# Performance work log

Measured on AMD Instinct MI355X. Metric: run time of the kernel, lower is better.

Reference implementation:

```python
import jax, jax.numpy as jnp
import numpy as np

N, D = 262144, 64
C, K, NSPLITS = 16, 4 + 12, 4  # K=16 codewords per codebook (2**NSPLITS)
K = 16
M = 16


def setup_inputs() -> dict:
    key = jax.random.key(0)
    k1, k2, k3, k4, k5 = jax.random.split(key, 5)
    A = jax.random.normal(k1, (N, D), dtype=jnp.float32)
    B = jax.random.normal(k2, (M, D), dtype=jnp.float32)
    prototypes = jax.random.normal(k3, (C, K, D), dtype=jnp.float32)
    split_dims = jax.random.randint(k4, (C, NSPLITS), 0, D, dtype=jnp.int32)
    # level i of the binary tree uses 2**i thresholds; pad to 2**(NSPLITS-1)=8
    split_vals = jax.random.normal(k5, (C, NSPLITS, 2 ** (NSPLITS - 1)), dtype=jnp.float32)
    return {"A": A, "B": B, "prototypes": prototypes,
            "split_dims": split_dims, "split_vals": split_vals}


def _encode(A, split_dims, split_vals):
    # Vectorized maddness_encode / apply_hash_function over all C codebooks.
    n = A.shape[0]
    c = split_dims.shape[0]
    nsplits = split_dims.shape[1]
    c_idx = jnp.arange(c)[None, :]                      # [1, C]
    group_ids = jnp.zeros((n, c), dtype=jnp.int32)      # [N, C]
    for i in range(nsplits):                            # fixed tiny loop (4 levels)
        x = A[:, split_dims[:, i]]                      # [N, C] gather of split dim
        vals_i = split_vals[:, i, :]                    # [C, 8]
        v = vals_i[c_idx, group_ids]                    # [N, C] per-group threshold
        group_ids = group_ids * 2 + (x > v).astype(jnp.int32)
    return group_ids                                    # [N, C] in [0, K)


def reference(A, B, prototypes, split_dims, split_vals):
    # 1) encode A rows: binary-tree hash per codebook -> codeword ids
    A_enc = _encode(A, split_dims, split_vals)          # [N, C] int32
    # 2) LUTs: luts[m, c, k] = <B[m], prototypes[c, k]>  (maddness_lut per row)
    luts = jnp.einsum('md,ckd->ckm', B, prototypes)     # [C, K, M]
    # 3) LUT-based accumulate (quantize_lut=False path): sum over codebooks
    c_idx = jnp.arange(luts.shape[0])[None, :]          # [1, C]
    g = luts[c_idx, A_enc]                              # [N, C, M] gathered LUT entries
    out = g.sum(axis=1).T                               # [M, N]
    return out
```

## Files before the change

### kernel.cpp

```cpp
#include <hip/hip_runtime.h>
#include <hip/hip_fp16.h>


#define NROWS 262144
#define DDIM  64
#define RSTR  65
#define LSTR  24
#define EBLK  4096
#define ABLK  1024

typedef __attribute__((ext_vector_type(8))) _Float16 half8;
typedef __attribute__((ext_vector_type(4))) unsigned int u32x4;

__global__ __launch_bounds__(64) void encode_kernel(
    const float* __restrict__ A,
    const float* __restrict__ B,
    const float* __restrict__ P,
    const int*   __restrict__ sd,
    const float* __restrict__ sv,
    _Float16* __restrict__ lutw,
    uint2* __restrict__ codes)
{
    __shared__ float rows_s[64 * RSTR];
    __shared__ float sv_s[512];
    const int t = threadIdx.x;

    ((float4*)sv_s)[t]      = ((const float4*)sv)[t];
    ((float4*)sv_s)[t + 64] = ((const float4*)sv)[t + 64];

    const float4* A4 = (const float4*)A;
    long base = (long)blockIdx.x * (64 * DDIM / 4);
    float4 R[16];
    #pragma unroll
    for (int j = 0; j < 16; ++j) R[j] = A4[base + j * 64 + t];

    if (blockIdx.x < 16) {
        const int m = t & 15;
        const float4* Bp = (const float4*)(B + m * DDIM);
        float4 brow[16];
        #pragma unroll
        for (int q = 0; q < 16; ++q) brow[q] = Bp[q];
        #pragma unroll
        for (int i = 0; i < 4; ++i) {
            int o  = blockIdx.x * 256 + i * 64 + t;
            int ck = o >> 4;
            const float4* Pp = (const float4*)(P + ck * DDIM);
            float dot = 0.f;
            #pragma unroll
            for (int q = 0; q < 16; ++q) {
                float4 p = Pp[q];
                dot += p.x * brow[q].x + p.y * brow[q].y
                     + p.z * brow[q].z + p.w * brow[q].w;
            }
            lutw[o] = (_Float16)dot;
        }
    }

    #pragma unroll
    for (int j = 0; j < 16; ++j) {
        int f    = j * 64 + t;
        int row  = f >> 4;
        int colq = (f & 15) * 4;
        float* dst = &rows_s[row * RSTR + colq];
        dst[0] = R[j].x; dst[1] = R[j].y; dst[2] = R[j].z; dst[3] = R[j].w;
    }
    __syncthreads();

    const float* rrow = &rows_s[t * RSTR];
    unsigned int lo = 0, hi = 0;
    #pragma unroll
    for (int c = 0; c < 16; ++c) {
        const int sd0 = sd[c*4+0], sd1 = sd[c*4+1];
        const int sd2 = sd[c*4+2], sd3 = sd[c*4+3];
        float x0 = rrow[sd0];
        float x1 = rrow[sd1];
        float x2 = rrow[sd2];
        float x3 = rrow[sd3];
        int g = (x0 > sv_s[c*32]) ? 1 : 0;
        g = (g << 1) | ((x1 > sv_s[c*32 +  8 + g]) ? 1 : 0);
        g = (g << 1) | ((x2 > sv_s[c*32 + 16 + g]) ? 1 : 0);
        g = (g << 1) | ((x3 > sv_s[c*32 + 24 + g]) ? 1 : 0);
        if (c < 8) lo |= (unsigned)g << (4 * c);
        else       hi |= (unsigned)g << (4 * (c - 8));
    }
    codes[blockIdx.x * 64 + t] = make_uint2(lo, hi);
}

__global__ __launch_bounds__(256) void accum_kernel(
    const uint2* __restrict__ codes,
    const _Float16* __restrict__ lutw,
    float* __restrict__ out)
{
    __shared__ __align__(16) _Float16 lut_s[256 * LSTR];
    const int t = threadIdx.x;

    {
        const u32x4* src = (const u32x4*)(lutw + t * 16);
        u32x4 q0 = src[0], q1 = src[1];
        *(u32x4*)(lut_s + t * LSTR)     = q0;
        *(u32x4*)(lut_s + t * LSTR + 8) = q1;
    }
    __syncthreads();

    const int n = blockIdx.x * 256 + t;
    const uint2 code = codes[n];

    half8 aE0 = {0,0,0,0,0,0,0,0}, aE1 = {0,0,0,0,0,0,0,0};
    half8 aO0 = {0,0,0,0,0,0,0,0}, aO1 = {0,0,0,0,0,0,0,0};

    #pragma unroll
    for (int c = 0; c < 8; ++c) {
        int g = (code.x >> (4 * c)) & 15;
        const _Float16* lp = lut_s + (c * 16 + g) * LSTR;
        half8 l0 = *(const half8*)(lp);
        half8 l1 = *(const half8*)(lp + 8);
        if (c & 1) { aO0 += l0; aO1 += l1; }
        else       { aE0 += l0; aE1 += l1; }
    }
    #pragma unroll
    for (int c = 8; c < 16; ++c) {
        int g = (code.y >> (4 * (c - 8))) & 15;
        const _Float16* lp = lut_s + (c * 16 + g) * LSTR;
        half8 l0 = *(const half8*)(lp);
        half8 l1 = *(const half8*)(lp + 8);
        if (c & 1) { aO0 += l0; aO1 += l1; }
        else       { aE0 += l0; aE1 += l1; }
    }

    #pragma unroll
    for (int m = 0; m < 8; ++m) {
        out[(long)m       * NROWS + n] = (float)aE0[m] + (float)aO0[m];
        out[(long)(m + 8) * NROWS + n] = (float)aE1[m] + (float)aO1[m];
    }
}

extern "C" void kernel_launch(void* const* d_in, const int* in_sizes, int n_in,
                              void* d_out, int out_size, void* d_ws, size_t ws_size,
                              hipStream_t stream) {
    const float* A  = (const float*)d_in[0];
    const float* B  = (const float*)d_in[1];
    const float* P  = (const float*)d_in[2];
    const int*   sd = (const int*)d_in[3];
    const float* sv = (const float*)d_in[4];
    float* out = (float*)d_out;

    _Float16* lutw = (_Float16*)d_ws;
    uint2*    codes = (uint2*)((char*)d_ws + 8192);

    encode_kernel<<<dim3(EBLK), dim3(64), 0, stream>>>(A, B, P, sd, sv, lutw, codes);
    accum_kernel<<<dim3(ABLK), dim3(256), 0, stream>>>(codes, lutw, out);
}
```

Measured before the change: 109.7 us.

## Process two row tiles per encode block with prefetch and branchless threshold selection

Each encode block now handles 128 rows in two 64-row tiles. The second tile's global loads are issued while the first tile is being encoded, which halves the grid. Threshold lookup changes from data-dependent indexed LDS reads to vectorized loads followed by selects, and the accum kernel issues its code load before the LUT staging barrier. The cost is higher register pressure from holding two 16-float4 buffers, plus extra barriers per block.

Measured after the change: 111.5 us. Within noise of the previous version (+1.6%).

```diff
diff --git a/kernel.cpp b/kernel.cpp
--- a/kernel.cpp
+++ b/kernel.cpp
@@ -6,11 +6,64 @@
 #define DDIM  64
 #define RSTR  65
 #define LSTR  24
-#define EBLK  4096
+#define EBLK  2048
 #define ABLK  1024
 
 typedef __attribute__((ext_vector_type(8))) _Float16 half8;
 typedef __attribute__((ext_vector_type(4))) unsigned int u32x4;
+
+__device__ __forceinline__ void scatter_tile(const float4* R, float* rows_s, int t) {
+    #pragma unroll
+    for (int j = 0; j < 16; ++j) {
+        int f    = j * 64 + t;
+        int row  = f >> 4;
+        int colq = (f & 15) * 4;
+        float* dst = &rows_s[row * RSTR + colq];
+        dst[0] = R[j].x; dst[1] = R[j].y; dst[2] = R[j].z; dst[3] = R[j].w;
+    }
+}
+
+__device__ __forceinline__ void encode_tile(
+    const float* rows_s, const float* sv_s, const int* __restrict__ sd,
+    int t, unsigned int& lo, unsigned int& hi)
+{
+    const float* rrow = &rows_s[t * RSTR];
+    lo = 0; hi = 0;
+    #pragma unroll
+    for (int c = 0; c < 16; ++c) {
+        const int sd0 = sd[c*4+0], sd1 = sd[c*4+1];
+        const int sd2 = sd[c*4+2], sd3 = sd[c*4+3];
+        float x0 = rrow[sd0];
+        float x1 = rrow[sd1];
+        float x2 = rrow[sd2];
+        float x3 = rrow[sd3];
+
+        const float* svc = &sv_s[c * 32];
+        float  v1  = svc[0];
+        float2 v2  = *(const float2*)(svc + 8);
+        float4 v3  = *(const float4*)(svc + 16);
+        float4 v4a = *(const float4*)(svc + 24);
+        float4 v4b = *(const float4*)(svc + 28);
+
+        bool b0 = x0 > v1;
+        float v2s = b0 ? v2.y : v2.x;
+        bool b1 = x1 > v2s;
+        float v3hi = b1 ? v3.w : v3.z;
+        float v3lo = b1 ? v3.y : v3.x;
+        float v3s  = b0 ? v3hi : v3lo;
+        bool b2 = x2 > v3s;
+        float4 v4  = b0 ? v4b : v4a;
+        float v4hi = b2 ? v4.w : v4.z;
+        float v4lo = b2 ? v4.y : v4.x;
+        float v4s  = b1 ? v4hi : v4lo;
+        bool b3 = x3 > v4s;
+
+        unsigned int g = ((((((unsigned)b0 << 1) | (unsigned)b1) << 1)
+                           | (unsigned)b2) << 1) | (unsigned)b3;
+        if (c < 8) lo |= g << (4 * c);
+        else       hi |= g << (4 * (c - 8));
+    }
+}
 
 __global__ __launch_bounds__(64) void encode_kernel(
     const float* __restrict__ A,
@@ -22,17 +75,17 @@
     uint2* __restrict__ codes)
 {
     __shared__ float rows_s[64 * RSTR];
-    __shared__ float sv_s[512];
+    __shared__ __align__(16) float sv_s[512];
     const int t = threadIdx.x;
+
+    const float4* A4 = (const float4*)A;
+    const long base0 = (long)blockIdx.x * (128 * DDIM / 4);
+    float4 R0[16];
+    #pragma unroll
+    for (int j = 0; j < 16; ++j) R0[j] = A4[base0 + j * 64 + t];
 
     ((float4*)sv_s)[t]      = ((const float4*)sv)[t];
     ((float4*)sv_s)[t + 64] = ((const float4*)sv)[t + 64];
-
-    const float4* A4 = (const float4*)A;
-    long base = (long)blockIdx.x * (64 * DDIM / 4);
-    float4 R[16];
-    #pragma unroll
-    for (int j = 0; j < 16; ++j) R[j] = A4[base + j * 64 + t];
 
     if (blockIdx.x < 16) {
         const int m = t & 15;
@@ -56,34 +109,24 @@
         }
     }
 
-    #pragma unroll
-    for (int j = 0; j < 16; ++j) {
-        int f    = j * 64 + t;
-        int row  = f >> 4;
-        int colq = (f & 15) * 4;
-        float* dst = &rows_s[row * RSTR + colq];
-        dst[0] = R[j].x; dst[1] = R[j].y; dst[2] = R[j].z; dst[3] = R[j].w;
-    }
+    scatter_tile(R0, rows_s, t);
     __syncthreads();
 
-    const float* rrow = &rows_s[t * RSTR];
-    unsigned int lo = 0, hi = 0;
+    float4 R1[16];
     #pragma unroll
-    for (int c = 0; c < 16; ++c) {
-        const int sd0 = sd[c*4+0], sd1 = sd[c*4+1];
-        const int sd2 = sd[c*4+2], sd3 = sd[c*4+3];
-        float x0 = rrow[sd0];
-        float x1 = rrow[sd1];
-        float x2 = rrow[sd2];
-        float x3 = rrow[sd3];
-        int g = (x0 > sv_s[c*32]) ? 1 : 0;
-        g = (g << 1) | ((x1 > sv_s[c*32 +  8 + g]) ? 1 : 0);
-        g = (g << 1) | ((x2 > sv_s[c*32 + 16 + g]) ? 1 : 0);
-        g = (g << 1) | ((x3 > sv_s[c*32 + 24 + g]) ? 1 : 0);
-        if (c < 8) lo |= (unsigned)g << (4 * c);
-        else       hi |= (unsigned)g << (4 * (c - 8));
-    }
-    codes[blockIdx.x * 64 + t] = make_uint2(lo, hi);
+    for (int j = 0; j < 16; ++j) R1[j] = A4[base0 + 1024 + j * 64 + t];
+
+    unsigned int lo0, hi0;
+    encode_tile(rows_s, sv_s, sd, t, lo0, hi0);
+    codes[blockIdx.x * 128 + t] = make_uint2(lo0, hi0);
+
+    __syncthreads();
+    scatter_tile(R1, rows_s, t);
+    __syncthreads();
+
+    unsigned int lo1, hi1;
+    encode_tile(rows_s, sv_s, sd, t, lo1, hi1);
+    codes[blockIdx.x * 128 + 64 + t] = make_uint2(lo1, hi1);
 }
 
 __global__ __launch_bounds__(256) void accum_kernel(
@@ -94,6 +137,9 @@
     __shared__ __align__(16) _Float16 lut_s[256 * LSTR];
     const int t = threadIdx.x;
 
+    const int n = blockIdx.x * 256 + t;
+    const uint2 code = codes[n];
+
     {
         const u32x4* src = (const u32x4*)(lutw + t * 16);
         u32x4 q0 = src[0], q1 = src[1];
@@ -101,9 +147,6 @@
         *(u32x4*)(lut_s + t * LSTR + 8) = q1;
     }
     __syncthreads();
-
-    const int n = blockIdx.x * 256 + t;
-    const uint2 code = codes[n];
 
     half8 aE0 = {0,0,0,0,0,0,0,0}, aE1 = {0,0,0,0,0,0,0,0};
     half8 aO0 = {0,0,0,0,0,0,0,0}, aO1 = {0,0,0,0,0,0,0,0};
```
